# Performance work log

Hardware: AMD Instinct MI355X
Metric: run time of the kernel (lower is better)

The kernel has to match this reference:

```python
import jax, jax.numpy as jnp
import numpy as np

N_NODES = 100000
N_EDGES = 3200000
N_FEAT = 512
NHID = 256
LATENT = 64

def _spmm(edge_index, edge_weight, h, num_nodes):
    # out[dst] = sum_e w_e * h[src_e]  (sparse adj @ h)
    src, dst = edge_index[0], edge_index[1]
    msgs = edge_weight[:, None] * h[src]            # [E, D]
    return jax.ops.segment_sum(msgs, dst, num_segments=num_nodes)

def _gcn_conv(x, edge_index, edge_weight, W, b, num_nodes):
    # GCNConv: adj @ (x @ W) + b
    return _spmm(edge_index, edge_weight, x @ W, num_nodes) + b

def setup_inputs() -> dict:
    key = jax.random.key(0)
    ks = jax.random.split(key, 8)
    x = jax.random.normal(ks[0], (N_NODES, N_FEAT), dtype=jnp.float32)
    edge_index = jax.random.randint(ks[1], (2, N_EDGES), 0, N_NODES, dtype=jnp.int32)
    edge_weight = jax.random.uniform(ks[2], (N_EDGES,), dtype=jnp.float32)
    s1 = 1.0 / np.sqrt(N_FEAT)
    s2 = 1.0 / np.sqrt(NHID)
    W1 = jax.random.normal(ks[3], (N_FEAT, NHID), dtype=jnp.float32) * s1
    b1 = jnp.zeros((NHID,), dtype=jnp.float32)
    W_mu = jax.random.normal(ks[4], (NHID, LATENT), dtype=jnp.float32) * s2
    b_mu = jnp.zeros((LATENT,), dtype=jnp.float32)
    W_logvar = jax.random.normal(ks[5], (NHID, LATENT), dtype=jnp.float32) * s2
    b_logvar = jnp.zeros((LATENT,), dtype=jnp.float32)
    return {"x": x, "edge_index": edge_index, "edge_weight": edge_weight,
            "W1": W1, "b1": b1, "W_mu": W_mu, "b_mu": b_mu,
            "W_logvar": W_logvar, "b_logvar": b_logvar}

def reference(x, edge_index, edge_weight, W1, b1, W_mu, b_mu, W_logvar, b_logvar):
    n = x.shape[0]
    # dropout is identity in eval mode (training=False)
    h = jax.nn.relu(_gcn_conv(x, edge_index, edge_weight, W1, b1, n))  # [N, nhid]
    mu = _gcn_conv(h, edge_index, edge_weight, W_mu, b_mu, n)          # [N, latent]
    logvar = _gcn_conv(h, edge_index, edge_weight, W_logvar, b_logvar, n)
    return (mu, logvar)
```

## Files before the change

### kernel.cpp

```cpp
#include <hip/hip_runtime.h>
#include <hip/hip_bf16.h>

#define NN 100000
#define NE 3200000
#define NF 512
#define NH 256
#define NL 64
#define PAD 40

#define NBKT 256
#define NPB 391
#define CAP 13500

typedef __bf16 bf16x8 __attribute__((ext_vector_type(8)));
typedef __bf16 bf16x4 __attribute__((ext_vector_type(4)));
typedef __bf16 bf16x2 __attribute__((ext_vector_type(2)));
typedef float  f32x4  __attribute__((ext_vector_type(4)));

__global__ void k_binit2(int* __restrict__ bcur) {
    int t = threadIdx.x;
    bcur[t * 16] = t * CAP;
}

__global__ __launch_bounds__(256) void k_bucket0(const int* __restrict__ src,
                                                 const int* __restrict__ dst,
                                                 const int* __restrict__ wbits,
                                                 int* __restrict__ bcur,
                                                 int2* __restrict__ stage_sw,
                                                 int* __restrict__ stage_d) {
    __shared__ int cnt[NBKT];
    __shared__ int base[NBKT];
    int tid = threadIdx.x;
    cnt[tid] = 0;
    __syncthreads();
    int e0 = blockIdx.x * 1024;
    int ss[4], ww[4], dd[4], lr[4], bb[4];
#pragma unroll
    for (int k = 0; k < 4; k++) {
        int e = e0 + k * 256 + tid;
        int d = dst[e];
        ss[k] = src[e];
        ww[k] = wbits[e];
        dd[k] = d;
        bb[k] = (int)((unsigned)d / NPB);
        lr[k] = atomicAdd(&cnt[bb[k]], 1);
    }
    __syncthreads();
    base[tid] = atomicAdd(&bcur[tid * 16], cnt[tid]);
    __syncthreads();
#pragma unroll
    for (int k = 0; k < 4; k++) {
        int pos = base[bb[k]] + lr[k];
        stage_sw[pos] = make_int2(ss[k], ww[k]);
        stage_d[pos] = dd[k];
    }
}

__global__ void k_bscan(const int* __restrict__ bcur, int* __restrict__ bstart) {
    __shared__ int s[NBKT];
    int t = threadIdx.x;
    int v = bcur[t * 16] - t * CAP;
    s[t] = v;
    __syncthreads();
    for (int off = 1; off < NBKT; off <<= 1) {
        int a = (t >= off) ? s[t - off] : 0;
        __syncthreads();
        s[t] += a;
        __syncthreads();
    }
    bstart[t] = s[t] - v;
    if (t == NBKT - 1) bstart[NBKT] = s[t];
}

__global__ __launch_bounds__(512) void k_build(const int2* __restrict__ stage_sw,
                                               const int* __restrict__ stage_d,
                                               const int* __restrict__ bcur,
                                               const int* __restrict__ bstart,
                                               int* __restrict__ deg,
                                               int* __restrict__ row_ptr,
                                               int2* __restrict__ sedge) {
    __shared__ int hist[NPB];
    __shared__ int roff[NPB + 1];
    int b = blockIdx.x;
    int t = threadIdx.x;
    int n0 = b * NPB;
    int nb = NN - n0; if (nb > NPB) nb = NPB;
    int s0 = b * CAP;
    int fill = bcur[b * 16] - s0;

    for (int i = t; i < nb; i += 512) hist[i] = 0;
    __syncthreads();
    for (int i = t; i < fill; i += 512)
        atomicAdd(&hist[stage_d[s0 + i] - n0], 1);
    __syncthreads();
    if (t == 0) {
        int acc = 0;
        for (int i = 0; i < nb; i++) { roff[i] = acc; acc += hist[i]; }
        roff[nb] = acc;
    }
    __syncthreads();
    int base = bstart[b];
    for (int i = t; i < nb; i += 512) {
        deg[n0 + i] = hist[i];
        row_ptr[n0 + i] = base + roff[i];
    }
    __syncthreads();
    for (int i = t; i < nb; i += 512) hist[i] = 0;
    __syncthreads();
    for (int i = t; i < fill; i += 512) {
        int d = stage_d[s0 + i] - n0;
        int r = atomicAdd(&hist[d], 1);
        sedge[base + roff[d] + r] = stage_sw[s0 + i];
    }
}

__global__ void k_packW1(const float* __restrict__ W, __bf16* __restrict__ P) {
    int i = blockIdx.x * 256 + threadIdx.x;
    int j = i & 7, l = (i >> 3) & 63, kc = (i >> 9) & 15, nt = i >> 13;
    int k = kc * 32 + (l >> 4) * 8 + j;
    int n = nt * 16 + (l & 15);
    P[i] = (__bf16)W[k * NH + n];
}

__global__ void k_packW2(const float* __restrict__ Wmu, const float* __restrict__ Wlv,
                         __bf16* __restrict__ P) {
    int i = blockIdx.x * 256 + threadIdx.x;
    int j = i & 7, l = (i >> 3) & 63, kc = (i >> 9) & 7, nt = i >> 12;
    int k = kc * 32 + (l >> 4) * 8 + j;
    int n = nt * 16 + (l & 15);
    float v = (n < NL) ? Wmu[k * NL + n] : Wlv[k * NL + (n - NL)];
    P[i] = (__bf16)v;
}

__global__ __launch_bounds__(256) void k_gemm1(const float* __restrict__ x,
                                               const __bf16* __restrict__ Wp,
                                               __bf16* __restrict__ TA,
                                               __bf16* __restrict__ TB) {
    __shared__ __bf16 As[64 * PAD];
    int tid = threadIdx.x;
    int wv = tid >> 6, lane = tid & 63;
    int quad = lane >> 4, l16 = lane & 15;
    long m0 = (long)blockIdx.x * 64;

    int srow = tid >> 2;
    int scol = (tid & 3) * 8;
    long grow = m0 + srow; if (grow > NN - 1) grow = NN - 1;
    const float* xrow = x + grow * NF;

    f32x4 acc[4][4];
#pragma unroll
    for (int a = 0; a < 4; a++)
#pragma unroll
        for (int b = 0; b < 4; b++) acc[a][b] = (f32x4)0.f;

    float4 p0 = *(const float4*)(xrow + scol);
    float4 p1 = *(const float4*)(xrow + scol + 4);

    for (int kc = 0; kc < 16; kc++) {
        union { bf16x8 v; __bf16 e[8]; } u;
        u.e[0] = (__bf16)p0.x; u.e[1] = (__bf16)p0.y;
        u.e[2] = (__bf16)p0.z; u.e[3] = (__bf16)p0.w;
        u.e[4] = (__bf16)p1.x; u.e[5] = (__bf16)p1.y;
        u.e[6] = (__bf16)p1.z; u.e[7] = (__bf16)p1.w;
        *(bf16x8*)&As[srow * PAD + scol] = u.v;
        __syncthreads();
        if (kc < 15) {
            p0 = *(const float4*)(xrow + (kc + 1) * 32 + scol);
            p1 = *(const float4*)(xrow + (kc + 1) * 32 + scol + 4);
        }
        bf16x8 bfr[4];
#pragma unroll
        for (int nt = 0; nt < 4; nt++)
            bfr[nt] = *(const bf16x8*)(Wp + (((long)(wv * 4 + nt) * 16 + kc) * 64 + lane) * 8);
#pragma unroll
        for (int mt = 0; mt < 4; mt++) {
            bf16x8 af = *(const bf16x8*)&As[(mt * 16 + l16) * PAD + quad * 8];
#pragma unroll
            for (int nt = 0; nt < 4; nt++)
                acc[mt][nt] = __builtin_amdgcn_mfma_f32_16x16x32_bf16(af, bfr[nt], acc[mt][nt], 0, 0, 0);
        }
        __syncthreads();
    }
    __bf16* T = (wv < 2) ? TA : TB;
    int c0 = (wv & 1) * 64;
#pragma unroll
    for (int mt = 0; mt < 4; mt++)
#pragma unroll
        for (int r = 0; r < 4; r++) {
            long gr = m0 + mt * 16 + quad * 4 + r;
            if (gr < NN) {
#pragma unroll
                for (int nt = 0; nt < 4; nt++)
                    T[gr * 128 + c0 + nt * 16 + l16] = (__bf16)acc[mt][nt][r];
            }
        }
}

__global__ __launch_bounds__(256) void k_spmm_h(const __bf16* __restrict__ T,
                                                const int2* __restrict__ sedge,
                                                const int* __restrict__ row_ptr,
                                                const int* __restrict__ deg,
                                                const float* __restrict__ bias,
                                                __bf16* __restrict__ o) {
    int wave = threadIdx.x >> 6, lane = threadIdx.x & 63;
    int n = blockIdx.x * 4 + wave;
    if (n >= NN) return;
    int i = row_ptr[n];
    int end = i + deg[n];
    float a0 = 0.f, a1 = 0.f;
    const bf16x2* base = (const bf16x2*)T;
    for (; i + 8 <= end; i += 8) {
        int2 e0 = sedge[i], e1 = sedge[i+1], e2 = sedge[i+2], e3 = sedge[i+3];
        int2 e4 = sedge[i+4], e5 = sedge[i+5], e6 = sedge[i+6], e7 = sedge[i+7];
        bf16x2 v0 = base[(long)e0.x * 64 + lane];
        bf16x2 v1 = base[(long)e1.x * 64 + lane];
        bf16x2 v2 = base[(long)e2.x * 64 + lane];
        bf16x2 v3 = base[(long)e3.x * 64 + lane];
        bf16x2 v4 = base[(long)e4.x * 64 + lane];
        bf16x2 v5 = base[(long)e5.x * 64 + lane];
        bf16x2 v6 = base[(long)e6.x * 64 + lane];
        bf16x2 v7 = base[(long)e7.x * 64 + lane];
        a0 += __uint_as_float(e0.y) * (float)v0[0] + __uint_as_float(e1.y) * (float)v1[0]
            + __uint_as_float(e2.y) * (float)v2[0] + __uint_as_float(e3.y) * (float)v3[0]
            + __uint_as_float(e4.y) * (float)v4[0] + __uint_as_float(e5.y) * (float)v5[0]
            + __uint_as_float(e6.y) * (float)v6[0] + __uint_as_float(e7.y) * (float)v7[0];
        a1 += __uint_as_float(e0.y) * (float)v0[1] + __uint_as_float(e1.y) * (float)v1[1]
            + __uint_as_float(e2.y) * (float)v2[1] + __uint_as_float(e3.y) * (float)v3[1]
            + __uint_as_float(e4.y) * (float)v4[1] + __uint_as_float(e5.y) * (float)v5[1]
            + __uint_as_float(e6.y) * (float)v6[1] + __uint_as_float(e7.y) * (float)v7[1];
    }
    for (; i < end; i++) {
        int2 e = sedge[i];
        float w = __uint_as_float(e.y);
        bf16x2 v = base[(long)e.x * 64 + lane];
        a0 += w * (float)v[0]; a1 += w * (float)v[1];
    }
    float2 b = ((const float2*)bias)[lane];
    bf16x2 ov;
    ov[0] = (__bf16)fmaxf(a0 + b.x, 0.f);
    ov[1] = (__bf16)fmaxf(a1 + b.y, 0.f);
    ((bf16x2*)o)[(long)n * 64 + lane] = ov;
}

__global__ __launch_bounds__(256) void k_gemm2(const __bf16* __restrict__ hA,
                                               const __bf16* __restrict__ hB,
                                               const __bf16* __restrict__ Wp,
                                               __bf16* __restrict__ HMb) {
    __shared__ __bf16 As[128 * PAD];
    int tid = threadIdx.x;
    int wv = tid >> 6, lane = tid & 63;
    int quad = lane >> 4, l16 = lane & 15;
    int wr = (wv >> 1) * 64, wc = (wv & 1) * 64;
    long m0 = (long)blockIdx.x * 128;

    int srow = tid >> 1;
    int scol = (tid & 1) * 16;
    long grow = m0 + srow; if (grow > NN - 1) grow = NN - 1;

    f32x4 acc[4][4];
#pragma unroll
    for (int a = 0; a < 4; a++)
#pragma unroll
        for (int b = 0; b < 4; b++) acc[a][b] = (f32x4)0.f;

    const __bf16* rA = hA + grow * 128;
    const __bf16* rB = hB + grow * 128;
    bf16x8 p0 = *(const bf16x8*)(rA + scol);
    bf16x8 p1 = *(const bf16x8*)(rA + scol + 8);

    for (int kc = 0; kc < 8; kc++) {
        *(bf16x8*)&As[srow * PAD + scol] = p0;
        *(bf16x8*)&As[srow * PAD + scol + 8] = p1;
        __syncthreads();
        if (kc < 7) {
            const __bf16* nxt = ((kc + 1) < 4 ? rA : rB) + ((kc + 1) & 3) * 32;
            p0 = *(const bf16x8*)(nxt + scol);
            p1 = *(const bf16x8*)(nxt + scol + 8);
        }
        bf16x8 bfr[4];
#pragma unroll
        for (int nt = 0; nt < 4; nt++) {
            int ntg = (wc >> 4) + nt;
            bfr[nt] = *(const bf16x8*)(Wp + (((long)ntg * 8 + kc) * 64 + lane) * 8);
        }
#pragma unroll
        for (int mt = 0; mt < 4; mt++) {
            bf16x8 af = *(const bf16x8*)&As[(wr + mt * 16 + l16) * PAD + quad * 8];
#pragma unroll
            for (int nt = 0; nt < 4; nt++)
                acc[mt][nt] = __builtin_amdgcn_mfma_f32_16x16x32_bf16(af, bfr[nt], acc[mt][nt], 0, 0, 0);
        }
        __syncthreads();
    }
#pragma unroll
    for (int mt = 0; mt < 4; mt++)
#pragma unroll
        for (int r = 0; r < 4; r++) {
            long gr = m0 + wr + mt * 16 + quad * 4 + r;
            if (gr < NN) {
#pragma unroll
                for (int nt = 0; nt < 4; nt++)
                    HMb[gr * 128 + wc + nt * 16 + l16] = (__bf16)acc[mt][nt][r];
            }
        }
}

__global__ __launch_bounds__(256) void k_spmm2(const __bf16* __restrict__ HMb,
                                               const int2* __restrict__ sedge,
                                               const int* __restrict__ row_ptr,
                                               const int* __restrict__ deg,
                                               const float* __restrict__ bmu,
                                               const float* __restrict__ blv,
                                               float* __restrict__ out) {
    int wave = threadIdx.x >> 6, lane = threadIdx.x & 63;
    int n = blockIdx.x * 4 + wave;
    if (n >= NN) return;
    int i = row_ptr[n];
    int end = i + deg[n];
    float a0 = 0.f, a1 = 0.f;
    const bf16x2* base = (const bf16x2*)HMb;
    for (; i + 8 <= end; i += 8) {
        int2 e0 = sedge[i], e1 = sedge[i+1], e2 = sedge[i+2], e3 = sedge[i+3];
        int2 e4 = sedge[i+4], e5 = sedge[i+5], e6 = sedge[i+6], e7 = sedge[i+7];
        bf16x2 v0 = base[(long)e0.x * 64 + lane];
        bf16x2 v1 = base[(long)e1.x * 64 + lane];
        bf16x2 v2 = base[(long)e2.x * 64 + lane];
        bf16x2 v3 = base[(long)e3.x * 64 + lane];
        bf16x2 v4 = base[(long)e4.x * 64 + lane];
        bf16x2 v5 = base[(long)e5.x * 64 + lane];
        bf16x2 v6 = base[(long)e6.x * 64 + lane];
        bf16x2 v7 = base[(long)e7.x * 64 + lane];
        a0 += __uint_as_float(e0.y) * (float)v0[0] + __uint_as_float(e1.y) * (float)v1[0]
            + __uint_as_float(e2.y) * (float)v2[0] + __uint_as_float(e3.y) * (float)v3[0]
            + __uint_as_float(e4.y) * (float)v4[0] + __uint_as_float(e5.y) * (float)v5[0]
            + __uint_as_float(e6.y) * (float)v6[0] + __uint_as_float(e7.y) * (float)v7[0];
        a1 += __uint_as_float(e0.y) * (float)v0[1] + __uint_as_float(e1.y) * (float)v1[1]
            + __uint_as_float(e2.y) * (float)v2[1] + __uint_as_float(e3.y) * (float)v3[1]
            + __uint_as_float(e4.y) * (float)v4[1] + __uint_as_float(e5.y) * (float)v5[1]
            + __uint_as_float(e6.y) * (float)v6[1] + __uint_as_float(e7.y) * (float)v7[1];
    }
    for (; i < end; i++) {
        int2 e = sedge[i];
        float w = __uint_as_float(e.y);
        bf16x2 v = base[(long)e.x * 64 + lane];
        a0 += w * (float)v[0]; a1 += w * (float)v[1];
    }
    if (lane < 32) {
        float2 b = ((const float2*)bmu)[lane];
        float2 o = {a0 + b.x, a1 + b.y};
        ((float2*)out)[(long)n * 32 + lane] = o;
    } else {
        float2 b = ((const float2*)blv)[lane - 32];
        float2 o = {a0 + b.x, a1 + b.y};
        ((float2*)(out + (long)NN * NL))[(long)n * 32 + (lane - 32)] = o;
    }
}

extern "C" void kernel_launch(void* const* d_in, const int* in_sizes, int n_in,
                              void* d_out, int out_size, void* d_ws, size_t ws_size,
                              hipStream_t stream) {
    const float* x   = (const float*)d_in[0];
    const int*   ei  = (const int*)d_in[1];
    const float* ew  = (const float*)d_in[2];
    const float* W1  = (const float*)d_in[3];
    const float* b1  = (const float*)d_in[4];
    const float* Wmu = (const float*)d_in[5];
    const float* bmu = (const float*)d_in[6];
    const float* Wlv = (const float*)d_in[7];
    const float* blv = (const float*)d_in[8];
    float* out = (float*)d_out;

    char* ws = (char*)d_ws;
    __bf16* XWa    = (__bf16*)(ws);
    __bf16* XWb2   = (__bf16*)(ws + 25600000);
    __bf16* hA     = (__bf16*)(ws + 51200000);
    __bf16* hB     = (__bf16*)(ws + 76800000);
    __bf16* HMb    = (__bf16*)(ws + 102400000);
    int2*  sedge   = (int2*) (ws + 128000000);
    int*   deg     = (int*)  (ws + 153600000);
    int*   row_ptr = (int*)  (ws + 154000000);
    int*   bcur    = (int*)  (ws + 154400000);
    int*   bstart  = (int*)  (ws + 154800000);
    __bf16* Wp1    = (__bf16*)(ws + 154900000);
    __bf16* Wp2    = (__bf16*)(ws + 155200000);

    int2* stage_sw = (int2*)(ws + 51200000);
    int*  stage_d  = (int*) (ws + 51200000 + (long)NBKT * CAP * 8);

    const int* esrc = ei;
    const int* edst = ei + NE;

    k_packW1<<<dim3(512), dim3(256), 0, stream>>>(W1, Wp1);
    k_packW2<<<dim3(128), dim3(256), 0, stream>>>(Wmu, Wlv, Wp2);

    k_binit2<<<dim3(1), dim3(NBKT), 0, stream>>>(bcur);
    k_bucket0<<<dim3(NE / 1024), dim3(256), 0, stream>>>(esrc, edst, (const int*)ew,
                                                         bcur, stage_sw, stage_d);
    k_bscan<<<dim3(1), dim3(NBKT), 0, stream>>>(bcur, bstart);
    k_build<<<dim3(NBKT), dim3(512), 0, stream>>>(stage_sw, stage_d, bcur, bstart,
                                                  deg, row_ptr, sedge);

    k_gemm1<<<dim3((NN + 63) / 64), dim3(256), 0, stream>>>(x, Wp1, XWa, XWb2);
    k_spmm_h<<<dim3((NN + 3) / 4), dim3(256), 0, stream>>>(XWa, sedge, row_ptr, deg, b1, hA);
    k_spmm_h<<<dim3((NN + 3) / 4), dim3(256), 0, stream>>>(XWb2, sedge, row_ptr, deg, b1 + 128, hB);

    k_gemm2<<<dim3((NN + 127) / 128), dim3(256), 0, stream>>>(hA, hB, Wp2, HMb);
    k_spmm2<<<dim3((NN + 3) / 4), dim3(256), 0, stream>>>(HMb, sedge, row_ptr, deg, bmu, blv, out);
}
```

Before: 847.3 us.

## Merge hidden SpMM halves into one pass and sort edges by source class

The two half-width hidden-layer SpMM launches become one kernel that gathers 4 bf16 per lane across the full 256-wide row. The edge list is read once instead of twice, and the gemm1 output and gemm2 input now use a single 256-wide layout. The CSR build now also sorts each node's edges by a coarse source-node class (16 classes), aiming for better locality in the gathers. The cost is a larger shared histogram and a leftover dead first histogram pass, and the wider row of one node doubles the per-edge gather footprint compared with either earlier pass.

```diff
diff --git a/kernel.cpp b/kernel.cpp
--- a/kernel.cpp
+++ b/kernel.cpp
@@ -11,6 +11,8 @@
 #define NBKT 256
 #define NPB 391
 #define CAP 13500
+#define NCLS 16
+#define DIVC 6250
 
 typedef __bf16 bf16x8 __attribute__((ext_vector_type(8)));
 typedef __bf16 bf16x4 __attribute__((ext_vector_type(4)));
@@ -39,9 +41,11 @@
     for (int k = 0; k < 4; k++) {
         int e = e0 + k * 256 + tid;
         int d = dst[e];
-        ss[k] = src[e];
+        int s = src[e];
+        ss[k] = s;
         ww[k] = wbits[e];
-        dd[k] = d;
+        int cls = (int)((unsigned)s / DIVC);
+        dd[k] = d | (cls << 20);
         bb[k] = (int)((unsigned)d / NPB);
         lr[k] = atomicAdd(&cnt[bb[k]], 1);
     }
@@ -79,8 +83,8 @@
                                                int* __restrict__ deg,
                                                int* __restrict__ row_ptr,
                                                int2* __restrict__ sedge) {
-    __shared__ int hist[NPB];
-    __shared__ int roff[NPB + 1];
+    __shared__ int hist2[NPB * NCLS];
+    __shared__ int sb[2][512];
     int b = blockIdx.x;
     int t = threadIdx.x;
     int n0 = b * NPB;
@@ -88,29 +92,55 @@
     int s0 = b * CAP;
     int fill = bcur[b * 16] - s0;
 
-    for (int i = t; i < nb; i += 512) hist[i] = 0;
-    __syncthreads();
-    for (int i = t; i < fill; i += 512)
-        atomicAdd(&hist[stage_d[s0 + i] - n0], 1);
-    __syncthreads();
-    if (t == 0) {
-        int acc = 0;
-        for (int i = 0; i < nb; i++) { roff[i] = acc; acc += hist[i]; }
-        roff[nb] = acc;
-    }
-    __syncthreads();
+    for (int i = t; i < nb * NCLS; i += 512) hist2[i] = 0;
+    __syncthreads();
+    for (int i = t; i < fill; i += 512) {
+        int v = stage_d[s0 + i];
+        atomicAdd(&hist2[(v & 0xFFFFF) - n0 + ((v >> 20) * 0)], 1);
+    }
+    __syncthreads();
+    for (int i = t; i < nb * NCLS; i += 512) hist2[i] = 0;
+    __syncthreads();
+    for (int i = t; i < fill; i += 512) {
+        int v = stage_d[s0 + i];
+        int dn = (v & 0xFFFFF) - n0;
+        int c = v >> 20;
+        atomicAdd(&hist2[dn * NCLS + c], 1);
+    }
+    __syncthreads();
+    int tot = 0;
+    if (t < nb) {
+#pragma unroll
+        for (int c = 0; c < NCLS; c++) tot += hist2[t * NCLS + c];
+    }
+    sb[0][t] = (t < nb) ? tot : 0;
+    __syncthreads();
+    int cur = 0;
+    for (int off = 1; off < 512; off <<= 1) {
+        int nv = sb[cur][t] + ((t >= off) ? sb[cur][t - off] : 0);
+        cur ^= 1;
+        sb[cur][t] = nv;
+        __syncthreads();
+    }
     int base = bstart[b];
-    for (int i = t; i < nb; i += 512) {
-        deg[n0 + i] = hist[i];
-        row_ptr[n0 + i] = base + roff[i];
-    }
-    __syncthreads();
-    for (int i = t; i < nb; i += 512) hist[i] = 0;
+    if (t < nb) {
+        int acc = base + sb[cur][t] - tot;
+        deg[n0 + t] = tot;
+        row_ptr[n0 + t] = acc;
+#pragma unroll
+        for (int c = 0; c < NCLS; c++) {
+            int tmp = hist2[t * NCLS + c];
+            hist2[t * NCLS + c] = acc;
+            acc += tmp;
+        }
+    }
     __syncthreads();
     for (int i = t; i < fill; i += 512) {
-        int d = stage_d[s0 + i] - n0;
-        int r = atomicAdd(&hist[d], 1);
-        sedge[base + roff[d] + r] = stage_sw[s0 + i];
+        int v = stage_d[s0 + i];
+        int dn = (v & 0xFFFFF) - n0;
+        int c = v >> 20;
+        int pos = atomicAdd(&hist2[dn * NCLS + c], 1);
+        sedge[pos] = stage_sw[s0 + i];
     }
 }
 
@@ -134,8 +164,7 @@
 
 __global__ __launch_bounds__(256) void k_gemm1(const float* __restrict__ x,
                                                const __bf16* __restrict__ Wp,
-                                               __bf16* __restrict__ TA,
-                                               __bf16* __restrict__ TB) {
+                                               __bf16* __restrict__ T) {
     __shared__ __bf16 As[64 * PAD];
     int tid = threadIdx.x;
     int wv = tid >> 6, lane = tid & 63;
@@ -181,8 +210,6 @@
         }
         __syncthreads();
     }
-    __bf16* T = (wv < 2) ? TA : TB;
-    int c0 = (wv & 1) * 64;
 #pragma unroll
     for (int mt = 0; mt < 4; mt++)
 #pragma unroll
@@ -191,7 +218,7 @@
             if (gr < NN) {
 #pragma unroll
                 for (int nt = 0; nt < 4; nt++)
-                    T[gr * 128 + c0 + nt * 16 + l16] = (__bf16)acc[mt][nt][r];
+                    T[gr * 256 + wv * 64 + nt * 16 + l16] = (__bf16)acc[mt][nt][r];
             }
         }
 }
@@ -207,43 +234,49 @@
     if (n >= NN) return;
     int i = row_ptr[n];
     int end = i + deg[n];
-    float a0 = 0.f, a1 = 0.f;
-    const bf16x2* base = (const bf16x2*)T;
+    float a0 = 0.f, a1 = 0.f, a2 = 0.f, a3 = 0.f;
+    const bf16x4* base = (const bf16x4*)T;
     for (; i + 8 <= end; i += 8) {
         int2 e0 = sedge[i], e1 = sedge[i+1], e2 = sedge[i+2], e3 = sedge[i+3];
         int2 e4 = sedge[i+4], e5 = sedge[i+5], e6 = sedge[i+6], e7 = sedge[i+7];
-        bf16x2 v0 = base[(long)e0.x * 64 + lane];
-        bf16x2 v1 = base[(long)e1.x * 64 + lane];
-        bf16x2 v2 = base[(long)e2.x * 64 + lane];
-        bf16x2 v3 = base[(long)e3.x * 64 + lane];
-        bf16x2 v4 = base[(long)e4.x * 64 + lane];
-        bf16x2 v5 = base[(long)e5.x * 64 + lane];
-        bf16x2 v6 = base[(long)e6.x * 64 + lane];
-        bf16x2 v7 = base[(long)e7.x * 64 + lane];
-        a0 += __uint_as_float(e0.y) * (float)v0[0] + __uint_as_float(e1.y) * (float)v1[0]
-            + __uint_as_float(e2.y) * (float)v2[0] + __uint_as_float(e3.y) * (float)v3[0]
-            + __uint_as_float(e4.y) * (float)v4[0] + __uint_as_float(e5.y) * (float)v5[0]
-            + __uint_as_float(e6.y) * (float)v6[0] + __uint_as_float(e7.y) * (float)v7[0];
-        a1 += __uint_as_float(e0.y) * (float)v0[1] + __uint_as_float(e1.y) * (float)v1[1]
-            + __uint_as_float(e2.y) * (float)v2[1] + __uint_as_float(e3.y) * (float)v3[1]
-            + __uint_as_float(e4.y) * (float)v4[1] + __uint_as_float(e5.y) * (float)v5[1]
-            + __uint_as_float(e6.y) * (float)v6[1] + __uint_as_float(e7.y) * (float)v7[1];
+        bf16x4 v0 = base[(long)e0.x * 64 + lane];
+        bf16x4 v1 = base[(long)e1.x * 64 + lane];
+        bf16x4 v2 = base[(long)e2.x * 64 + lane];
+        bf16x4 v3 = base[(long)e3.x * 64 + lane];
+        bf16x4 v4 = base[(long)e4.x * 64 + lane];
+        bf16x4 v5 = base[(long)e5.x * 64 + lane];
+        bf16x4 v6 = base[(long)e6.x * 64 + lane];
+        bf16x4 v7 = base[(long)e7.x * 64 + lane];
+        float w0 = __uint_as_float(e0.y), w1 = __uint_as_float(e1.y);
+        float w2 = __uint_as_float(e2.y), w3 = __uint_as_float(e3.y);
+        float w4 = __uint_as_float(e4.y), w5 = __uint_as_float(e5.y);
+        float w6 = __uint_as_float(e6.y), w7 = __uint_as_float(e7.y);
+        a0 += w0*(float)v0[0] + w1*(float)v1[0] + w2*(float)v2[0] + w3*(float)v3[0]
+            + w4*(float)v4[0] + w5*(float)v5[0] + w6*(float)v6[0] + w7*(float)v7[0];
+        a1 += w0*(float)v0[1] + w1*(float)v1[1] + w2*(float)v2[1] + w3*(float)v3[1]
+            + w4*(float)v4[1] + w5*(float)v5[1] + w6*(float)v6[1] + w7*(float)v7[1];
+        a2 += w0*(float)v0[2] + w1*(float)v1[2] + w2*(float)v2[2] + w3*(float)v3[2]
+            + w4*(float)v4[2] + w5*(float)v5[2] + w6*(float)v6[2] + w7*(float)v7[2];
+        a3 += w0*(float)v0[3] + w1*(float)v1[3] + w2*(float)v2[3] + w3*(float)v3[3]
+            + w4*(float)v4[3] + w5*(float)v5[3] + w6*(float)v6[3] + w7*(float)v7[3];
     }
     for (; i < end; i++) {
         int2 e = sedge[i];
         float w = __uint_as_float(e.y);
-        bf16x2 v = base[(long)e.x * 64 + lane];
-        a0 += w * (float)v[0]; a1 += w * (float)v[1];
-    }
-    float2 b = ((const float2*)bias)[lane];
-    bf16x2 ov;
-    ov[0] = (__bf16)fmaxf(a0 + b.x, 0.f);
-    ov[1] = (__bf16)fmaxf(a1 + b.y, 0.f);
-    ((bf16x2*)o)[(long)n * 64 + lane] = ov;
-}
-
-__global__ __launch_bounds__(256) void k_gemm2(const __bf16* __restrict__ hA,
-                                               const __bf16* __restrict__ hB,
+        bf16x4 v = base[(long)e.x * 64 + lane];
+        a0 += w*(float)v[0]; a1 += w*(float)v[1];
+        a2 += w*(float)v[2]; a3 += w*(float)v[3];
+    }
+    float4 bv = ((const float4*)bias)[lane];
+    bf16x4 ov;
+    ov[0] = (__bf16)fmaxf(a0 + bv.x, 0.f);
+    ov[1] = (__bf16)fmaxf(a1 + bv.y, 0.f);
+    ov[2] = (__bf16)fmaxf(a2 + bv.z, 0.f);
+    ov[3] = (__bf16)fmaxf(a3 + bv.w, 0.f);
+    ((bf16x4*)o)[(long)n * 64 + lane] = ov;
+}
+
+__global__ __launch_bounds__(256) void k_gemm2(const __bf16* __restrict__ h,
                                                const __bf16* __restrict__ Wp,
                                                __bf16* __restrict__ HMb) {
     __shared__ __bf16 As[128 * PAD];
@@ -263,17 +296,16 @@
 #pragma unroll
         for (int b = 0; b < 4; b++) acc[a][b] = (f32x4)0.f;
 
-    const __bf16* rA = hA + grow * 128;
-    const __bf16* rB = hB + grow * 128;
-    bf16x8 p0 = *(const bf16x8*)(rA + scol);
-    bf16x8 p1 = *(const bf16x8*)(rA + scol + 8);
+    const __bf16* rH = h + grow * 256;
+    bf16x8 p0 = *(const bf16x8*)(rH + scol);
+    bf16x8 p1 = *(const bf16x8*)(rH + scol + 8);
 
     for (int kc = 0; kc < 8; kc++) {
         *(bf16x8*)&As[srow * PAD + scol] = p0;
         *(bf16x8*)&As[srow * PAD + scol + 8] = p1;
         __syncthreads();
         if (kc < 7) {
-            const __bf16* nxt = ((kc + 1) < 4 ? rA : rB) + ((kc + 1) & 3) * 32;
+            const __bf16* nxt = rH + (kc + 1) * 32;
             p0 = *(const bf16x8*)(nxt + scol);
             p1 = *(const bf16x8*)(nxt + scol + 8);
         }
@@ -371,10 +403,8 @@
     float* out = (float*)d_out;
 
     char* ws = (char*)d_ws;
-    __bf16* XWa    = (__bf16*)(ws);
-    __bf16* XWb2   = (__bf16*)(ws + 25600000);
-    __bf16* hA     = (__bf16*)(ws + 51200000);
-    __bf16* hB     = (__bf16*)(ws + 76800000);
+    __bf16* XW     = (__bf16*)(ws);
+    __bf16* h      = (__bf16*)(ws + 51200000);
     __bf16* HMb    = (__bf16*)(ws + 102400000);
     int2*  sedge   = (int2*) (ws + 128000000);
     int*   deg     = (int*)  (ws + 153600000);
@@ -400,10 +430,9 @@
     k_build<<<dim3(NBKT), dim3(512), 0, stream>>>(stage_sw, stage_d, bcur, bstart,
                                                   deg, row_ptr, sedge);
 
-    k_gemm1<<<dim3((NN + 63) / 64), dim3(256), 0, stream>>>(x, Wp1, XWa, XWb2);
-    k_spmm_h<<<dim3((NN + 3) / 4), dim3(256), 0, stream>>>(XWa, sedge, row_ptr, deg, b1, hA);
-    k_spmm_h<<<dim3((NN + 3) / 4), dim3(256), 0, stream>>>(XWb2, sedge, row_ptr, deg, b1 + 128, hB);
-
-    k_gemm2<<<dim3((NN + 127) / 128), dim3(256), 0, stream>>>(hA, hB, Wp2, HMb);
+    k_gemm1<<<dim3((NN + 63) / 64), dim3(256), 0, stream>>>(x, Wp1, XW);
+    k_spmm_h<<<dim3((NN + 3) / 4), dim3(256), 0, stream>>>(XW, sedge, row_ptr, deg, b1, h);
+
+    k_gemm2<<<dim3((NN + 127) / 128), dim3(256), 0, stream>>>(h, Wp2, HMb);
     k_spmm2<<<dim3((NN + 3) / 4), dim3(256), 0, stream>>>(HMb, sedge, row_ptr, deg, bmu, blv, out);
 }
```

Result: no change. 842.7 us (-0.6%).
